# Kernel optimization log

Measured on AMD Instinct MI355X. Metric: run time of the kernel, lower is better.

Reference implementation:

```python
import jax, jax.numpy as jnp
import numpy as np

B, T, IN, HID = 256, 512, 1024, 1024


def setup_inputs() -> dict:
    key = jax.random.key(0)
    ks = jax.random.split(key, 9)
    s = 1.0 / np.sqrt(IN + HID)
    def lin(k):
        kw, kb = jax.random.split(k)
        W = jax.random.uniform(kw, (IN + HID, HID), jnp.float32, -s, s)
        b = jax.random.uniform(kb, (HID,), jnp.float32, -s, s)
        return W, b
    Wf, bf = lin(ks[0])
    Wi, bi = lin(ks[1])
    Wo, bo = lin(ks[2])
    Wc, bc = lin(ks[3])
    x = jax.random.normal(ks[4], (B, T, IN), jnp.float32)
    return {"x": x, "Wf": Wf, "bf": bf, "Wi": Wi, "bi": bi,
            "Wo": Wo, "bo": bo, "Wc": Wc, "bc": bc}


def reference(x, Wf, bf, Wi, bi, Wo, bo, Wc, bc):
    # x: [B, T, IN]; returns final (h, c): each [B, HID]
    batch = x.shape[0]
    hid = Wf.shape[1]

    def step(carry, xt):
        h, c = carry
        comb = jnp.concatenate([xt, h], axis=1)      # [B, IN+HID]
        i = jax.nn.sigmoid(comb @ Wi + bi)
        f = jax.nn.sigmoid(comb @ Wf + bf)
        o = jax.nn.sigmoid(comb @ Wo + bo)
        g = jnp.tanh(comb @ Wc + bc)
        c_next = f * c + i * g
        h_next = o * jnp.tanh(c_next)
        return (h_next, c_next), None

    init = (jnp.zeros((batch, hid), x.dtype), jnp.zeros((batch, hid), x.dtype))
    (h, c), _ = jax.lax.scan(step, init, jnp.swapaxes(x, 0, 1))
    return (h, c)
```

## Files before the change

### kernel.cpp

```cpp
#include <hip/hip_runtime.h>
#include <hip/hip_bf16.h>

#define B_DIM 256
#define T_DIM 512
#define WINT 64
#define IN_DIM 1024
#define HID_DIM 1024
#define BLK 16384

typedef __attribute__((ext_vector_type(8))) short bf16x8;
typedef __attribute__((ext_vector_type(4))) float f32x4;

__device__ __forceinline__ unsigned short f2bf(float v) {
  unsigned int u = __float_as_uint(v);
  unsigned int r = (u + 0x7fffu + ((u >> 16) & 1u)) >> 16;
  return (unsigned short)r;
}
__device__ __forceinline__ float bflo(unsigned u) { return __uint_as_float(u << 16); }
__device__ __forceinline__ float bfhi(unsigned u) { return __uint_as_float(u & 0xffff0000u); }

typedef __attribute__((address_space(3))) unsigned int lds_uint;
typedef const __attribute__((address_space(1))) unsigned int g_uint;
__device__ __forceinline__ void gload_lds16(const void* g, void* l) {
  __builtin_amdgcn_global_load_lds((g_uint*)g, (lds_uint*)l, 16, 0, 0);
}
__device__ __forceinline__ void glds2(const unsigned char* s, unsigned char* d) {
  gload_lds16(s, d);
  gload_lds16(s + 1024, d + 1024);
}

#define WAITVM(N) asm volatile("s_waitcnt vmcnt(" #N ")" ::: "memory")

__global__ void prep_pack_w(const float* __restrict__ Wi, const float* __restrict__ Wf,
                            const float* __restrict__ Wo, const float* __restrict__ Wc,
                            unsigned char* __restrict__ Wp) {
  const int bid = blockIdx.x;
  const int cb = bid >> 4, kc = bid & 15;
  const int tid = threadIdx.x;
  const int col = tid & 63;
  const int g = col >> 4, h_in = col & 15;
  const int kq = tid >> 6;
  const float* W = (g == 0) ? Wi : (g == 1) ? Wf : (g == 2) ? Wo : Wc;
  const float* src = W + (size_t)(kc * 128 + kq * 32) * HID_DIM + cb * 16 + h_in;
  unsigned char* dst = Wp + (size_t)bid * BLK;
  const unsigned int xo = (unsigned int)((col & 7) << 4);
#pragma unroll
  for (int b4 = 0; b4 < 4; ++b4) {
    unsigned short u[8];
#pragma unroll
    for (int j = 0; j < 8; ++j)
      u[j] = f2bf(src[(size_t)(b4 * 8 + j) * HID_DIM]);
    uint4 pk;
    pk.x = (unsigned)u[0] | ((unsigned)u[1] << 16);
    pk.y = (unsigned)u[2] | ((unsigned)u[3] << 16);
    pk.z = (unsigned)u[4] | ((unsigned)u[5] << 16);
    pk.w = (unsigned)u[6] | ((unsigned)u[7] << 16);
    unsigned int byte = ((unsigned int)(col * 256 + kq * 64 + b4 * 16)) ^ xo;
    *(uint4*)(dst + byte) = pk;
  }
}

__global__ void prep_bias(const float* __restrict__ bi, const float* __restrict__ bf_,
                          const float* __restrict__ bo, const float* __restrict__ bc,
                          float* __restrict__ bp) {
  int p = blockIdx.x * 256 + threadIdx.x;
  int cbb = p >> 6, col = p & 63, g = col >> 4, h_in = col & 15;
  const float* b = (g == 0) ? bi : (g == 1) ? bf_ : (g == 2) ? bo : bc;
  bp[p] = b[cbb * 16 + h_in];
}

__global__ void prep_pack_x_win(const float* __restrict__ x,
                                unsigned char* __restrict__ xpw, int t0) {
  const int bid = blockIdx.x;
  const int kc = bid & 7, mb = (bid >> 3) & 3, tw = bid >> 5;
  const int tid = threadIdx.x;
  const int row = tid >> 2, kseg = tid & 3;
  const float* src = x + ((size_t)(mb * 64 + row) * T_DIM + (t0 + tw)) * IN_DIM +
                     kc * 128 + kseg * 32;
  unsigned char* dst = xpw + (size_t)bid * BLK;
  const unsigned int xo = (unsigned)((row & 7) << 4);
#pragma unroll
  for (int c4 = 0; c4 < 4; ++c4) {
    float4 f0 = *(const float4*)(src + c4 * 8);
    float4 f1 = *(const float4*)(src + c4 * 8 + 4);
    uint4 pk;
    pk.x = (unsigned)f2bf(f0.x) | ((unsigned)f2bf(f0.y) << 16);
    pk.y = (unsigned)f2bf(f0.z) | ((unsigned)f2bf(f0.w) << 16);
    pk.z = (unsigned)f2bf(f1.x) | ((unsigned)f2bf(f1.y) << 16);
    pk.w = (unsigned)f2bf(f1.z) | ((unsigned)f2bf(f1.w) << 16);
    *(uint4*)(dst + (((unsigned)(row * 256 + kseg * 64 + c4 * 16)) ^ xo)) = pk;
  }
}

__global__ __launch_bounds__(512, 2) void bulk_gx(
    const unsigned char* __restrict__ xpw, const unsigned char* __restrict__ Wq,
    unsigned char* __restrict__ gxw) {
  extern __shared__ unsigned char ring[];
  const int wg = blockIdx.x;
  const int cb = wg & 63, mb = (wg >> 6) & 3, tg = wg >> 8;
  const int tid = threadIdx.x, lane = tid & 63, w = tid >> 6;
  const int rg = w & 1, cg = (w >> 1) & 1, kh = w >> 2;
  const int fr = lane & 15;
  const unsigned koff2 = (unsigned)((lane >> 4) << 4);
  const int rsub = (lane >> 4) * 4;
  const int cl = cg * 32 + fr;

  bf16x8 Breg[4][2][4];
#pragma unroll
  for (int ci = 0; ci < 4; ++ci)
#pragma unroll
    for (int cbf = 0; cbf < 2; ++cbf)
#pragma unroll
      for (int ks = 0; ks < 4; ++ks) {
        const unsigned c2 = (unsigned)(cl + cbf * 16);
        Breg[ci][cbf][ks] = *(const bf16x8*)(
            Wq + ((size_t)(cb * 16 + kh * 4 + ci) << 14) +
            ((c2 * 256 + (unsigned)ks * 64 + koff2) ^ ((c2 & 7) << 4)));
      }

  float* gates = (float*)ring;
  unsigned char* dstb = ring + w * 2048;

#pragma unroll 1
  for (int i = 0; i < 16; ++i) {
    const int tl = tg * 16 + i;
    const unsigned char* xA =
        xpw + ((size_t)((tl * 4 + mb) * 8)) * BLK + w * 2048 + lane * 16;
    f32x4 acc[2][2] = {{{0.f,0.f,0.f,0.f},{0.f,0.f,0.f,0.f}},
                       {{0.f,0.f,0.f,0.f},{0.f,0.f,0.f,0.f}}};
#pragma unroll
    for (int c = 0; c < 4; ++c) glds2(xA + (size_t)c * BLK, dstb + c * 16384);
#pragma unroll
    for (int kc = 0; kc < 8; ++kc) {
      if (kc <= 4) WAITVM(6);
      else if (kc == 5) WAITVM(4);
      else if (kc == 6) WAITVM(2);
      else WAITVM(0);
      __builtin_amdgcn_s_barrier();
      if ((kc >> 2) == kh) {
        const unsigned char* Ab = ring + (kc & 3) * 16384;
#pragma unroll
        for (int ks = 0; ks < 4; ++ks) {
          const unsigned r0 = (unsigned)(rg * 32 + fr), r1 = r0 + 16;
          const unsigned kb = (unsigned)ks * 64 + koff2;
          bf16x8 a0 = *(const bf16x8*)(Ab + ((r0 * 256 + kb) ^ ((r0 & 7) << 4)));
          bf16x8 a1 = *(const bf16x8*)(Ab + ((r1 * 256 + kb) ^ ((r1 & 7) << 4)));
#pragma unroll
          for (int cbf = 0; cbf < 2; ++cbf) {
            acc[0][cbf] = __builtin_amdgcn_mfma_f32_16x16x32_bf16(
                a0, Breg[kc & 3][cbf][ks], acc[0][cbf], 0, 0, 0);
            acc[1][cbf] = __builtin_amdgcn_mfma_f32_16x16x32_bf16(
                a1, Breg[kc & 3][cbf][ks], acc[1][cbf], 0, 0, 0);
          }
        }
      }
      __builtin_amdgcn_s_barrier();
      if (kc + 4 < 8) glds2(xA + (size_t)(kc + 4) * BLK, dstb + ((kc + 4) & 3) * 16384);
    }
    if (kh == 0) {
#pragma unroll
      for (int rb = 0; rb < 2; ++rb)
#pragma unroll
        for (int cbf = 0; cbf < 2; ++cbf)
#pragma unroll
          for (int j = 0; j < 4; ++j)
            gates[(rg * 32 + rb * 16 + rsub + j) * 65 + cg * 32 + cbf * 16 + fr] =
                acc[rb][cbf][j];
    }
    __syncthreads();
    if (kh == 1) {
#pragma unroll
      for (int rb = 0; rb < 2; ++rb)
#pragma unroll
        for (int cbf = 0; cbf < 2; ++cbf)
#pragma unroll
          for (int j = 0; j < 4; ++j)
            gates[(rg * 32 + rb * 16 + rsub + j) * 65 + cg * 32 + cbf * 16 + fr] +=
                acc[rb][cbf][j];
    }
    __syncthreads();
    {
      const int erow = tid & 63, hb2 = (tid >> 6) * 2;
      uint4 pk;
      unsigned u[4];
#pragma unroll
      for (int g = 0; g < 4; ++g) {
        float lo = gates[erow * 65 + g * 16 + hb2];
        float hi = gates[erow * 65 + g * 16 + hb2 + 1];
        u[g] = (unsigned)f2bf(lo) | ((unsigned)f2bf(hi) << 16);
      }
      pk.x = u[0]; pk.y = u[1]; pk.z = u[2]; pk.w = u[3];
      *(uint4*)(gxw + ((size_t)((tl * 4 + mb) * 64 + cb)) * 8192 + (size_t)tid * 16) = pk;
    }
    __syncthreads();
  }
}

__global__ __launch_bounds__(512, 1) void lstm_seq(
    const unsigned char* __restrict__ gxw, const unsigned char* __restrict__ Wq,
    const float* __restrict__ bp, unsigned char* hring,
    unsigned int* flags, float* cst, float* __restrict__ out, int t0) {
  extern __shared__ unsigned char ring[];
  const int wg = blockIdx.x, mb = wg >> 6, cb = wg & 63;
  const int tid = threadIdx.x, lane = tid & 63, w = tid >> 6;
  const int cg = w & 3, kh = w >> 2;
  const int fr = lane & 15;
  const unsigned koff2 = (unsigned)((lane >> 4) << 4);
  const int rsub = (lane >> 4) * 4;
  const int cl = cg * 16 + fr;

  bf16x8 Breg[4][4];
#pragma unroll
  for (int kcl = 0; kcl < 4; ++kcl)
#pragma unroll
    for (int ks = 0; ks < 4; ++ks)
      Breg[kcl][ks] = *(const bf16x8*)(
          Wq + ((size_t)(cb * 16 + 8 + kh * 4 + kcl) << 14) +
          (((unsigned)cl * 256 + (unsigned)ks * 64 + koff2) ^ ((unsigned)((cl & 7) << 4))));
#pragma unroll
  for (int kcl = 0; kcl < 4; ++kcl)
#pragma unroll
    for (int ks = 0; ks < 4; ++ks)
      asm volatile("" : "+v"(Breg[kcl][ks]));

  const int erow = tid & 63, hb2 = (tid >> 6) * 2;
  const size_t gidx = (size_t)(mb * 64 + erow) * HID_DIM + cb * 16 + hb2;
  float bI[2], bF[2], bO[2], bG[2];
#pragma unroll
  for (int j = 0; j < 2; ++j) {
    bI[j] = bp[cb * 64 + hb2 + j];
    bF[j] = bp[cb * 64 + 16 + hb2 + j];
    bO[j] = bp[cb * 64 + 32 + hb2 + j];
    bG[j] = bp[cb * 64 + 48 + hb2 + j];
  }
  float cr[2] = {0.f, 0.f};
  if (t0 > 0) { float2 c2v = *(const float2*)(cst + gidx); cr[0] = c2v.x; cr[1] = c2v.y; }

  float* gates0 = (float*)ring;
  float* gates1 = (float*)(ring + 32768);

#pragma unroll 1
  for (int tt = 0; tt < WINT; ++tt) {
    const int t = t0 + tt;
#pragma unroll
    for (int kcl = 0; kcl < 4; ++kcl)
#pragma unroll
      for (int ks = 0; ks < 4; ++ks)
        asm volatile("" : "+v"(Breg[kcl][ks]));
    uint4 gxv = *(const uint4*)(gxw + ((size_t)((tt * 4 + mb) * 64 + cb)) * 8192 +
                                (size_t)tid * 16);
    f32x4 acc[4] = {{0.f,0.f,0.f,0.f},{0.f,0.f,0.f,0.f},
                    {0.f,0.f,0.f,0.f},{0.f,0.f,0.f,0.f}};
    if (t > 0) {
      if (w == 0) {
        unsigned int* fl = &flags[mb * 64 + lane];
        while (!__all(__hip_atomic_load(fl, __ATOMIC_RELAXED,
                                        __HIP_MEMORY_SCOPE_AGENT) >= (unsigned)t))
          __builtin_amdgcn_s_sleep(2);
        (void)__hip_atomic_load(fl, __ATOMIC_ACQUIRE,
                                __HIP_MEMORY_SCOPE_AGENT);
      }
      __syncthreads();
      const unsigned char* hA = hring + (size_t)((t + 2) % 3) * 524288 +
                                (size_t)(mb * 8) * BLK + w * 2048 + lane * 16;
#pragma unroll
      for (int c = 0; c < 8; ++c)
        glds2(hA + (size_t)c * BLK, ring + c * 16384 + w * 2048);
#pragma unroll
      for (int kc = 0; kc < 8; ++kc) {
        if (kc == 0) WAITVM(14);
        else if (kc == 1) WAITVM(12);
        else if (kc == 2) WAITVM(10);
        else if (kc == 3) WAITVM(8);
        else if (kc == 4) WAITVM(6);
        else if (kc == 5) WAITVM(4);
        else if (kc == 6) WAITVM(2);
        else WAITVM(0);
        __builtin_amdgcn_s_barrier();
        if ((kc >> 2) == kh) {
          const int kcl = kc & 3;
          const unsigned char* Ab = ring + kc * 16384;
#pragma unroll
          for (int ks = 0; ks < 4; ++ks) {
            const unsigned kb = (unsigned)ks * 64 + koff2;
#pragma unroll
            for (int rb = 0; rb < 4; ++rb) {
              const unsigned r0 = (unsigned)(rb * 16 + fr);
              bf16x8 a0 = *(const bf16x8*)(Ab + ((r0 * 256 + kb) ^ ((r0 & 7) << 4)));
              acc[rb] = __builtin_amdgcn_mfma_f32_16x16x32_bf16(
                  a0, Breg[kcl][ks], acc[rb], 0, 0, 0);
            }
          }
        }
      }
    }
    {
      float* gx_ = (kh == 0) ? gates0 : gates1;
#pragma unroll
      for (int rb = 0; rb < 4; ++rb)
#pragma unroll
        for (int j = 0; j < 4; ++j)
          gx_[(rb * 16 + rsub + j) * 65 + cg * 16 + fr] = acc[rb][j];
    }
    __syncthreads();
    float hv[2];
    {
      unsigned gu0 = gxv.x, gu1 = gxv.y, gu2 = gxv.z, gu3 = gxv.w;
#pragma unroll
      for (int j = 0; j < 2; ++j) {
        int hc = hb2 + j;
        float gx0 = j ? bfhi(gu0) : bflo(gu0);
        float gx1 = j ? bfhi(gu1) : bflo(gu1);
        float gx2 = j ? bfhi(gu2) : bflo(gu2);
        float gx3 = j ? bfhi(gu3) : bflo(gu3);
        float pi = gates0[erow * 65 + hc]      + gates1[erow * 65 + hc]      + bI[j] + gx0;
        float pf = gates0[erow * 65 + 16 + hc] + gates1[erow * 65 + 16 + hc] + bF[j] + gx1;
        float po = gates0[erow * 65 + 32 + hc] + gates1[erow * 65 + 32 + hc] + bO[j] + gx2;
        float pg = gates0[erow * 65 + 48 + hc] + gates1[erow * 65 + 48 + hc] + bG[j] + gx3;
        float ig = 1.f / (1.f + __expf(-pi));
        float fg = 1.f / (1.f + __expf(-pf));
        float og = 1.f / (1.f + __expf(-po));
        float gg = 1.f - 2.f / (1.f + __expf(2.f * pg));
        float cn = fg * cr[j] + ig * gg;
        cr[j] = cn;
        hv[j] = og * (1.f - 2.f / (1.f + __expf(2.f * cn)));
      }
    }
    if (t < T_DIM - 1) {
      int hcg = cb * 16 + hb2;
      int kc2 = hcg >> 7, kp = hcg & 127;
      unsigned byte = ((unsigned)(erow * 256 + kp * 2)) ^ ((unsigned)((erow & 7) << 4));
      unsigned pk = (unsigned)f2bf(hv[0]) | ((unsigned)f2bf(hv[1]) << 16);
      unsigned int* hd = (unsigned int*)(hring + (size_t)(t % 3) * 524288 +
                                         (size_t)(mb * 8 + kc2) * BLK + byte);
      __hip_atomic_store(hd, pk, __ATOMIC_RELAXED, __HIP_MEMORY_SCOPE_AGENT);
    }
    WAITVM(0);
    __syncthreads();
    if (tid == 0 && t < T_DIM - 1)
      __hip_atomic_store(&flags[mb * 64 + cb], (unsigned)(t + 1),
                         __ATOMIC_RELEASE, __HIP_MEMORY_SCOPE_AGENT);
    if (t == T_DIM - 1) {
      *(float2*)(out + gidx) = make_float2(hv[0], hv[1]);
      *(float2*)(out + (size_t)B_DIM * HID_DIM + gidx) = make_float2(cr[0], cr[1]);
    }
  }
  if (t0 + WINT < T_DIM) *(float2*)(cst + gidx) = make_float2(cr[0], cr[1]);
}

extern "C" void kernel_launch(void* const* d_in, const int* in_sizes, int n_in,
                              void* d_out, int out_size, void* d_ws, size_t ws_size,
                              hipStream_t stream) {
  (void)in_sizes; (void)n_in; (void)out_size;
  const float* x   = (const float*)d_in[0];
  const float* Wf_ = (const float*)d_in[1];
  const float* bf_ = (const float*)d_in[2];
  const float* Wi_ = (const float*)d_in[3];
  const float* bi_ = (const float*)d_in[4];
  const float* Wo_ = (const float*)d_in[5];
  const float* bo_ = (const float*)d_in[6];
  const float* Wc_ = (const float*)d_in[7];
  const float* bc_ = (const float*)d_in[8];
  float* out = (float*)d_out;
  unsigned char* ws = (unsigned char*)d_ws;

  unsigned char* Wp = ws;
  size_t off = 16777216;
  float* bp = (float*)(ws + off);                    off += 16384;
  unsigned int* flags = (unsigned int*)(ws + off);   off += 8192;
  unsigned int* consCnt = (unsigned int*)(ws + off); off += 8192;
  (void)consCnt;
  unsigned char* hring = ws + off;                   off += 3 * 524288;
  float* cst = (float*)(ws + off);                   off += 1048576;
  unsigned char* xpw = ws + off;                     off += (size_t)2048 * BLK;
  unsigned char* gxw = ws + off;                     off += (size_t)WINT * 256 * 8192;
  if (ws_size < off) return;

  prep_pack_w<<<1024, 256, 0, stream>>>(Wi_, Wf_, Wo_, Wc_, Wp);
  prep_bias<<<16, 256, 0, stream>>>(bi_, bf_, bo_, bc_, bp);
  hipMemsetAsync(flags, 0, 16384, stream);

  hipFuncSetAttribute((const void*)bulk_gx,
                      hipFuncAttributeMaxDynamicSharedMemorySize, 65536);
  hipFuncSetAttribute((const void*)lstm_seq,
                      hipFuncAttributeMaxDynamicSharedMemorySize, 131072);

  for (int t0 = 0; t0 < T_DIM; t0 += WINT) {
    prep_pack_x_win<<<2048, 256, 0, stream>>>(x, xpw, t0);
    bulk_gx<<<1024, 512, 65536, stream>>>(xpw, Wp, gxw);
    const unsigned char* a_gx = gxw;
    const unsigned char* a_wp = Wp;
    const float* a_bp = bp;
    unsigned char* a_hr = hring;
    unsigned int* a_fl = flags;
    float* a_cs = cst;
    float* a_out = out;
    int a_t0 = t0;
    void* args[] = {&a_gx, &a_wp, &a_bp, &a_hr, &a_fl, &a_cs, &a_out, &a_t0};
    hipLaunchCooperativeKernel((const void*)lstm_seq, dim3(256), dim3(512),
                               args, 131072u, stream);
  }
}
```

Before: 9.463 ms.

## Fuse input-projection GEMM with recurrent steps to overlap next window

Merges the bulk input-projection kernel and the sequential LSTM kernel into one kernel. In each cooperative launch, 256 blocks run the recurrent steps of the current window while another 256 blocks compute the input-gate GEMM for the next window into a double buffer. The window shrinks from 64 to 32 steps, and LDS per block is cut to 64KB so that two blocks can share a CU. This is meant to hide the input-projection cost behind the latency-bound recurrence. The risks are that the co-resident GEMM blocks compete with the recurrent blocks for CU time and memory bandwidth, that the recurrent path now uses a smaller 4-stage LDS ring, and that the extra windows add launch and synchronisation overhead.

```diff
diff --git a/kernel.cpp b/kernel.cpp
--- a/kernel.cpp
+++ b/kernel.cpp
@@ -3,7 +3,8 @@
 
 #define B_DIM 256
 #define T_DIM 512
-#define WINT 64
+#define WINT 32
+#define NWIN 16
 #define IN_DIM 1024
 #define HID_DIM 1024
 #define BLK 16384
@@ -92,44 +93,55 @@
   }
 }
 
-__global__ __launch_bounds__(512, 2) void bulk_gx(
-    const unsigned char* __restrict__ xpw, const unsigned char* __restrict__ Wq,
-    unsigned char* __restrict__ gxw) {
+__global__ __launch_bounds__(512, 4) void lstm_fused(
+    const unsigned char* __restrict__ gxCur, const unsigned char* __restrict__ xpNext,
+    const unsigned char* __restrict__ Wq, const float* __restrict__ bp,
+    unsigned char* __restrict__ gxNext, unsigned char* hring,
+    unsigned int* flags, float* cst, float* __restrict__ out,
+    int t0, int mode) {
   extern __shared__ unsigned char ring[];
-  const int wg = blockIdx.x;
-  const int cb = wg & 63, mb = (wg >> 6) & 3, tg = wg >> 8;
   const int tid = threadIdx.x, lane = tid & 63, w = tid >> 6;
-  const int rg = w & 1, cg = (w >> 1) & 1, kh = w >> 2;
+  const int cg = w & 3, kh = w >> 2;
   const int fr = lane & 15;
   const unsigned koff2 = (unsigned)((lane >> 4) << 4);
   const int rsub = (lane >> 4) * 4;
-  const int cl = cg * 32 + fr;
-
-  bf16x8 Breg[4][2][4];
-#pragma unroll
-  for (int ci = 0; ci < 4; ++ci)
-#pragma unroll
-    for (int cbf = 0; cbf < 2; ++cbf)
-#pragma unroll
-      for (int ks = 0; ks < 4; ++ks) {
-        const unsigned c2 = (unsigned)(cl + cbf * 16);
-        Breg[ci][cbf][ks] = *(const bf16x8*)(
-            Wq + ((size_t)(cb * 16 + kh * 4 + ci) << 14) +
-            ((c2 * 256 + (unsigned)ks * 64 + koff2) ^ ((c2 & 7) << 4)));
-      }
-
-  float* gates = (float*)ring;
-  unsigned char* dstb = ring + w * 2048;
-
-#pragma unroll 1
-  for (int i = 0; i < 16; ++i) {
-    const int tl = tg * 16 + i;
-    const unsigned char* xA =
-        xpw + ((size_t)((tl * 4 + mb) * 8)) * BLK + w * 2048 + lane * 16;
-    f32x4 acc[2][2] = {{{0.f,0.f,0.f,0.f},{0.f,0.f,0.f,0.f}},
-                       {{0.f,0.f,0.f,0.f},{0.f,0.f,0.f,0.f}}};
-#pragma unroll
-    for (int c = 0; c < 4; ++c) glds2(xA + (size_t)c * BLK, dstb + c * 16384);
+  const int cl = cg * 16 + fr;
+
+  bool isSeq; int wg;
+  if (mode == 0) {
+    isSeq = (int)blockIdx.x < 256;
+    wg = isSeq ? (int)blockIdx.x : (int)blockIdx.x - 256;
+  } else {
+    isSeq = (mode == 1);
+    wg = (int)blockIdx.x;
+  }
+  const int mb = (wg >> 6) & 3, cb = wg & 63;
+
+  bf16x8 Breg[4][4];
+  {
+    const int xoff = isSeq ? 8 : 0;
+#pragma unroll
+    for (int kcl = 0; kcl < 4; ++kcl)
+#pragma unroll
+      for (int ks = 0; ks < 4; ++ks)
+        Breg[kcl][ks] = *(const bf16x8*)(
+            Wq + ((size_t)(cb * 16 + xoff + kh * 4 + kcl) << 14) +
+            (((unsigned)cl * 256 + (unsigned)ks * 64 + koff2) ^
+             ((unsigned)((cl & 7) << 4))));
+#pragma unroll
+    for (int kcl = 0; kcl < 4; ++kcl)
+#pragma unroll
+      for (int ks = 0; ks < 4; ++ks)
+        asm volatile("" : "+v"(Breg[kcl][ks]));
+  }
+
+  float* gates0 = (float*)ring;
+  float* gates1 = (float*)(ring + 32768);
+
+  auto phases = [&](const unsigned char* Abase, f32x4* acc) {
+#pragma unroll
+    for (int c = 0; c < 4; ++c)
+      glds2(Abase + (size_t)c * BLK, ring + c * 16384 + w * 2048);
 #pragma unroll
     for (int kc = 0; kc < 8; ++kc) {
       if (kc <= 4) WAITVM(6);
@@ -138,214 +150,156 @@
       else WAITVM(0);
       __builtin_amdgcn_s_barrier();
       if ((kc >> 2) == kh) {
+        const int kcl = kc & 3;
         const unsigned char* Ab = ring + (kc & 3) * 16384;
 #pragma unroll
         for (int ks = 0; ks < 4; ++ks) {
-          const unsigned r0 = (unsigned)(rg * 32 + fr), r1 = r0 + 16;
           const unsigned kb = (unsigned)ks * 64 + koff2;
-          bf16x8 a0 = *(const bf16x8*)(Ab + ((r0 * 256 + kb) ^ ((r0 & 7) << 4)));
-          bf16x8 a1 = *(const bf16x8*)(Ab + ((r1 * 256 + kb) ^ ((r1 & 7) << 4)));
-#pragma unroll
-          for (int cbf = 0; cbf < 2; ++cbf) {
-            acc[0][cbf] = __builtin_amdgcn_mfma_f32_16x16x32_bf16(
-                a0, Breg[kc & 3][cbf][ks], acc[0][cbf], 0, 0, 0);
-            acc[1][cbf] = __builtin_amdgcn_mfma_f32_16x16x32_bf16(
-                a1, Breg[kc & 3][cbf][ks], acc[1][cbf], 0, 0, 0);
+#pragma unroll
+          for (int rb = 0; rb < 4; ++rb) {
+            const unsigned r0 = (unsigned)(rb * 16 + fr);
+            bf16x8 a0 = *(const bf16x8*)(Ab + ((r0 * 256 + kb) ^ ((r0 & 7) << 4)));
+            acc[rb] = __builtin_amdgcn_mfma_f32_16x16x32_bf16(
+                a0, Breg[kcl][ks], acc[rb], 0, 0, 0);
           }
         }
       }
       __builtin_amdgcn_s_barrier();
-      if (kc + 4 < 8) glds2(xA + (size_t)(kc + 4) * BLK, dstb + ((kc + 4) & 3) * 16384);
-    }
-    if (kh == 0) {
-#pragma unroll
-      for (int rb = 0; rb < 2; ++rb)
-#pragma unroll
-        for (int cbf = 0; cbf < 2; ++cbf)
+      if (kc + 4 < 8)
+        glds2(Abase + (size_t)(kc + 4) * BLK, ring + (kc & 3) * 16384 + w * 2048);
+    }
+  };
+
+  if (isSeq) {
+    const int erow = tid & 63, hb2 = (tid >> 6) * 2;
+    const size_t gidx = (size_t)(mb * 64 + erow) * HID_DIM + cb * 16 + hb2;
+    float bI[2], bF[2], bO[2], bG[2];
+#pragma unroll
+    for (int j = 0; j < 2; ++j) {
+      bI[j] = bp[cb * 64 + hb2 + j];
+      bF[j] = bp[cb * 64 + 16 + hb2 + j];
+      bO[j] = bp[cb * 64 + 32 + hb2 + j];
+      bG[j] = bp[cb * 64 + 48 + hb2 + j];
+    }
+    float cr[2] = {0.f, 0.f};
+    if (t0 > 0) { float2 c2v = *(const float2*)(cst + gidx); cr[0] = c2v.x; cr[1] = c2v.y; }
+
+#pragma unroll 1
+    for (int tt = 0; tt < WINT; ++tt) {
+      const int t = t0 + tt;
+#pragma unroll
+      for (int kcl = 0; kcl < 4; ++kcl)
+#pragma unroll
+        for (int ks = 0; ks < 4; ++ks)
+          asm volatile("" : "+v"(Breg[kcl][ks]));
+      uint4 gxv = *(const uint4*)(gxCur + ((size_t)((tt * 4 + mb) * 64 + cb)) * 8192 +
+                                  (size_t)tid * 16);
+      f32x4 acc[4] = {{0.f,0.f,0.f,0.f},{0.f,0.f,0.f,0.f},
+                      {0.f,0.f,0.f,0.f},{0.f,0.f,0.f,0.f}};
+      if (t > 0) {
+        if (w == 0) {
+          unsigned int* fl = &flags[mb * 64 + lane];
+          while (!__all(__hip_atomic_load(fl, __ATOMIC_RELAXED,
+                                          __HIP_MEMORY_SCOPE_AGENT) >= (unsigned)t))
+            __builtin_amdgcn_s_sleep(2);
+          (void)__hip_atomic_load(fl, __ATOMIC_ACQUIRE,
+                                  __HIP_MEMORY_SCOPE_AGENT);
+        }
+        __syncthreads();
+        const unsigned char* hA = hring + (size_t)((t + 2) % 3) * 524288 +
+                                  (size_t)(mb * 8) * BLK + w * 2048 + lane * 16;
+        phases(hA, acc);
+      }
+      {
+        float* g_ = kh ? gates1 : gates0;
+#pragma unroll
+        for (int rb = 0; rb < 4; ++rb)
 #pragma unroll
           for (int j = 0; j < 4; ++j)
-            gates[(rg * 32 + rb * 16 + rsub + j) * 65 + cg * 32 + cbf * 16 + fr] =
-                acc[rb][cbf][j];
-    }
-    __syncthreads();
-    if (kh == 1) {
-#pragma unroll
-      for (int rb = 0; rb < 2; ++rb)
-#pragma unroll
-        for (int cbf = 0; cbf < 2; ++cbf)
+            g_[(rb * 16 + rsub + j) * 65 + cg * 16 + fr] = acc[rb][j];
+      }
+      __syncthreads();
+      float hv[2];
+      {
+        unsigned gu0 = gxv.x, gu1 = gxv.y, gu2 = gxv.z, gu3 = gxv.w;
+#pragma unroll
+        for (int j = 0; j < 2; ++j) {
+          int hc = hb2 + j;
+          float gx0 = j ? bfhi(gu0) : bflo(gu0);
+          float gx1 = j ? bfhi(gu1) : bflo(gu1);
+          float gx2 = j ? bfhi(gu2) : bflo(gu2);
+          float gx3 = j ? bfhi(gu3) : bflo(gu3);
+          float pi = gates0[erow * 65 + hc]      + gates1[erow * 65 + hc]      + bI[j] + gx0;
+          float pf = gates0[erow * 65 + 16 + hc] + gates1[erow * 65 + 16 + hc] + bF[j] + gx1;
+          float po = gates0[erow * 65 + 32 + hc] + gates1[erow * 65 + 32 + hc] + bO[j] + gx2;
+          float pg = gates0[erow * 65 + 48 + hc] + gates1[erow * 65 + 48 + hc] + bG[j] + gx3;
+          float ig = 1.f / (1.f + __expf(-pi));
+          float fg = 1.f / (1.f + __expf(-pf));
+          float og = 1.f / (1.f + __expf(-po));
+          float gg = 1.f - 2.f / (1.f + __expf(2.f * pg));
+          float cn = fg * cr[j] + ig * gg;
+          cr[j] = cn;
+          hv[j] = og * (1.f - 2.f / (1.f + __expf(2.f * cn)));
+        }
+      }
+      if (t < T_DIM - 1) {
+        int hcg = cb * 16 + hb2;
+        int kc2 = hcg >> 7, kp = hcg & 127;
+        unsigned byte = ((unsigned)(erow * 256 + kp * 2)) ^ ((unsigned)((erow & 7) << 4));
+        unsigned pk = (unsigned)f2bf(hv[0]) | ((unsigned)f2bf(hv[1]) << 16);
+        unsigned int* hd = (unsigned int*)(hring + (size_t)(t % 3) * 524288 +
+                                           (size_t)(mb * 8 + kc2) * BLK + byte);
+        __hip_atomic_store(hd, pk, __ATOMIC_RELAXED, __HIP_MEMORY_SCOPE_AGENT);
+      }
+      WAITVM(0);
+      __syncthreads();
+      if (tid == 0 && t < T_DIM - 1)
+        __hip_atomic_store(&flags[mb * 64 + cb], (unsigned)(t + 1),
+                           __ATOMIC_RELEASE, __HIP_MEMORY_SCOPE_AGENT);
+      if (t == T_DIM - 1) {
+        *(float2*)(out + gidx) = make_float2(hv[0], hv[1]);
+        *(float2*)(out + (size_t)B_DIM * HID_DIM + gidx) = make_float2(cr[0], cr[1]);
+      }
+    }
+    if (t0 + WINT < T_DIM) *(float2*)(cst + gidx) = make_float2(cr[0], cr[1]);
+  } else {
+    const int erow = tid & 63, hb2 = (tid >> 6) * 2;
+#pragma unroll 1
+    for (int tl = 0; tl < WINT; ++tl) {
+#pragma unroll
+      for (int kcl = 0; kcl < 4; ++kcl)
+#pragma unroll
+        for (int ks = 0; ks < 4; ++ks)
+          asm volatile("" : "+v"(Breg[kcl][ks]));
+      f32x4 acc[4] = {{0.f,0.f,0.f,0.f},{0.f,0.f,0.f,0.f},
+                      {0.f,0.f,0.f,0.f},{0.f,0.f,0.f,0.f}};
+      const unsigned char* xA = xpNext + ((size_t)((tl * 4 + mb) * 8)) * BLK +
+                                w * 2048 + lane * 16;
+      phases(xA, acc);
+      {
+        float* g_ = kh ? gates1 : gates0;
+#pragma unroll
+        for (int rb = 0; rb < 4; ++rb)
 #pragma unroll
           for (int j = 0; j < 4; ++j)
-            gates[(rg * 32 + rb * 16 + rsub + j) * 65 + cg * 32 + cbf * 16 + fr] +=
-                acc[rb][cbf][j];
-    }
-    __syncthreads();
-    {
-      const int erow = tid & 63, hb2 = (tid >> 6) * 2;
-      uint4 pk;
-      unsigned u[4];
-#pragma unroll
-      for (int g = 0; g < 4; ++g) {
-        float lo = gates[erow * 65 + g * 16 + hb2];
-        float hi = gates[erow * 65 + g * 16 + hb2 + 1];
-        u[g] = (unsigned)f2bf(lo) | ((unsigned)f2bf(hi) << 16);
-      }
-      pk.x = u[0]; pk.y = u[1]; pk.z = u[2]; pk.w = u[3];
-      *(uint4*)(gxw + ((size_t)((tl * 4 + mb) * 64 + cb)) * 8192 + (size_t)tid * 16) = pk;
-    }
-    __syncthreads();
-  }
-}
-
-__global__ __launch_bounds__(512, 1) void lstm_seq(
-    const unsigned char* __restrict__ gxw, const unsigned char* __restrict__ Wq,
-    const float* __restrict__ bp, unsigned char* hring,
-    unsigned int* flags, float* cst, float* __restrict__ out, int t0) {
-  extern __shared__ unsigned char ring[];
-  const int wg = blockIdx.x, mb = wg >> 6, cb = wg & 63;
-  const int tid = threadIdx.x, lane = tid & 63, w = tid >> 6;
-  const int cg = w & 3, kh = w >> 2;
-  const int fr = lane & 15;
-  const unsigned koff2 = (unsigned)((lane >> 4) << 4);
-  const int rsub = (lane >> 4) * 4;
-  const int cl = cg * 16 + fr;
-
-  bf16x8 Breg[4][4];
-#pragma unroll
-  for (int kcl = 0; kcl < 4; ++kcl)
-#pragma unroll
-    for (int ks = 0; ks < 4; ++ks)
-      Breg[kcl][ks] = *(const bf16x8*)(
-          Wq + ((size_t)(cb * 16 + 8 + kh * 4 + kcl) << 14) +
-          (((unsigned)cl * 256 + (unsigned)ks * 64 + koff2) ^ ((unsigned)((cl & 7) << 4))));
-#pragma unroll
-  for (int kcl = 0; kcl < 4; ++kcl)
-#pragma unroll
-    for (int ks = 0; ks < 4; ++ks)
-      asm volatile("" : "+v"(Breg[kcl][ks]));
-
-  const int erow = tid & 63, hb2 = (tid >> 6) * 2;
-  const size_t gidx = (size_t)(mb * 64 + erow) * HID_DIM + cb * 16 + hb2;
-  float bI[2], bF[2], bO[2], bG[2];
-#pragma unroll
-  for (int j = 0; j < 2; ++j) {
-    bI[j] = bp[cb * 64 + hb2 + j];
-    bF[j] = bp[cb * 64 + 16 + hb2 + j];
-    bO[j] = bp[cb * 64 + 32 + hb2 + j];
-    bG[j] = bp[cb * 64 + 48 + hb2 + j];
-  }
-  float cr[2] = {0.f, 0.f};
-  if (t0 > 0) { float2 c2v = *(const float2*)(cst + gidx); cr[0] = c2v.x; cr[1] = c2v.y; }
-
-  float* gates0 = (float*)ring;
-  float* gates1 = (float*)(ring + 32768);
-
-#pragma unroll 1
-  for (int tt = 0; tt < WINT; ++tt) {
-    const int t = t0 + tt;
-#pragma unroll
-    for (int kcl = 0; kcl < 4; ++kcl)
-#pragma unroll
-      for (int ks = 0; ks < 4; ++ks)
-        asm volatile("" : "+v"(Breg[kcl][ks]));
-    uint4 gxv = *(const uint4*)(gxw + ((size_t)((tt * 4 + mb) * 64 + cb)) * 8192 +
-                                (size_t)tid * 16);
-    f32x4 acc[4] = {{0.f,0.f,0.f,0.f},{0.f,0.f,0.f,0.f},
-                    {0.f,0.f,0.f,0.f},{0.f,0.f,0.f,0.f}};
-    if (t > 0) {
-      if (w == 0) {
-        unsigned int* fl = &flags[mb * 64 + lane];
-        while (!__all(__hip_atomic_load(fl, __ATOMIC_RELAXED,
-                                        __HIP_MEMORY_SCOPE_AGENT) >= (unsigned)t))
-          __builtin_amdgcn_s_sleep(2);
-        (void)__hip_atomic_load(fl, __ATOMIC_ACQUIRE,
-                                __HIP_MEMORY_SCOPE_AGENT);
+            g_[(rb * 16 + rsub + j) * 65 + cg * 16 + fr] = acc[rb][j];
       }
       __syncthreads();
-      const unsigned char* hA = hring + (size_t)((t + 2) % 3) * 524288 +
-                                (size_t)(mb * 8) * BLK + w * 2048 + lane * 16;
-#pragma unroll
-      for (int c = 0; c < 8; ++c)
-        glds2(hA + (size_t)c * BLK, ring + c * 16384 + w * 2048);
-#pragma unroll
-      for (int kc = 0; kc < 8; ++kc) {
-        if (kc == 0) WAITVM(14);
-        else if (kc == 1) WAITVM(12);
-        else if (kc == 2) WAITVM(10);
-        else if (kc == 3) WAITVM(8);
-        else if (kc == 4) WAITVM(6);
-        else if (kc == 5) WAITVM(4);
-        else if (kc == 6) WAITVM(2);
-        else WAITVM(0);
-        __builtin_amdgcn_s_barrier();
-        if ((kc >> 2) == kh) {
-          const int kcl = kc & 3;
-          const unsigned char* Ab = ring + kc * 16384;
-#pragma unroll
-          for (int ks = 0; ks < 4; ++ks) {
-            const unsigned kb = (unsigned)ks * 64 + koff2;
-#pragma unroll
-            for (int rb = 0; rb < 4; ++rb) {
-              const unsigned r0 = (unsigned)(rb * 16 + fr);
-              bf16x8 a0 = *(const bf16x8*)(Ab + ((r0 * 256 + kb) ^ ((r0 & 7) << 4)));
-              acc[rb] = __builtin_amdgcn_mfma_f32_16x16x32_bf16(
-                  a0, Breg[kcl][ks], acc[rb], 0, 0, 0);
-            }
-          }
+      {
+        unsigned u[4];
+#pragma unroll
+        for (int g = 0; g < 4; ++g) {
+          float lo = gates0[erow * 65 + g * 16 + hb2] + gates1[erow * 65 + g * 16 + hb2];
+          float hi = gates0[erow * 65 + g * 16 + hb2 + 1] + gates1[erow * 65 + g * 16 + hb2 + 1];
+          u[g] = (unsigned)f2bf(lo) | ((unsigned)f2bf(hi) << 16);
         }
-      }
-    }
-    {
-      float* gx_ = (kh == 0) ? gates0 : gates1;
-#pragma unroll
-      for (int rb = 0; rb < 4; ++rb)
-#pragma unroll
-        for (int j = 0; j < 4; ++j)
-          gx_[(rb * 16 + rsub + j) * 65 + cg * 16 + fr] = acc[rb][j];
-    }
-    __syncthreads();
-    float hv[2];
-    {
-      unsigned gu0 = gxv.x, gu1 = gxv.y, gu2 = gxv.z, gu3 = gxv.w;
-#pragma unroll
-      for (int j = 0; j < 2; ++j) {
-        int hc = hb2 + j;
-        float gx0 = j ? bfhi(gu0) : bflo(gu0);
-        float gx1 = j ? bfhi(gu1) : bflo(gu1);
-        float gx2 = j ? bfhi(gu2) : bflo(gu2);
-        float gx3 = j ? bfhi(gu3) : bflo(gu3);
-        float pi = gates0[erow * 65 + hc]      + gates1[erow * 65 + hc]      + bI[j] + gx0;
-        float pf = gates0[erow * 65 + 16 + hc] + gates1[erow * 65 + 16 + hc] + bF[j] + gx1;
-        float po = gates0[erow * 65 + 32 + hc] + gates1[erow * 65 + 32 + hc] + bO[j] + gx2;
-        float pg = gates0[erow * 65 + 48 + hc] + gates1[erow * 65 + 48 + hc] + bG[j] + gx3;
-        float ig = 1.f / (1.f + __expf(-pi));
-        float fg = 1.f / (1.f + __expf(-pf));
-        float og = 1.f / (1.f + __expf(-po));
-        float gg = 1.f - 2.f / (1.f + __expf(2.f * pg));
-        float cn = fg * cr[j] + ig * gg;
-        cr[j] = cn;
-        hv[j] = og * (1.f - 2.f / (1.f + __expf(2.f * cn)));
-      }
-    }
-    if (t < T_DIM - 1) {
-      int hcg = cb * 16 + hb2;
-      int kc2 = hcg >> 7, kp = hcg & 127;
-      unsigned byte = ((unsigned)(erow * 256 + kp * 2)) ^ ((unsigned)((erow & 7) << 4));
-      unsigned pk = (unsigned)f2bf(hv[0]) | ((unsigned)f2bf(hv[1]) << 16);
-      unsigned int* hd = (unsigned int*)(hring + (size_t)(t % 3) * 524288 +
-                                         (size_t)(mb * 8 + kc2) * BLK + byte);
-      __hip_atomic_store(hd, pk, __ATOMIC_RELAXED, __HIP_MEMORY_SCOPE_AGENT);
-    }
-    WAITVM(0);
-    __syncthreads();
-    if (tid == 0 && t < T_DIM - 1)
-      __hip_atomic_store(&flags[mb * 64 + cb], (unsigned)(t + 1),
-                         __ATOMIC_RELEASE, __HIP_MEMORY_SCOPE_AGENT);
-    if (t == T_DIM - 1) {
-      *(float2*)(out + gidx) = make_float2(hv[0], hv[1]);
-      *(float2*)(out + (size_t)B_DIM * HID_DIM + gidx) = make_float2(cr[0], cr[1]);
-    }
-  }
-  if (t0 + WINT < T_DIM) *(float2*)(cst + gidx) = make_float2(cr[0], cr[1]);
+        uint4 pk; pk.x = u[0]; pk.y = u[1]; pk.z = u[2]; pk.w = u[3];
+        *(uint4*)(gxNext + ((size_t)((tl * 4 + mb) * 64 + cb)) * 8192 +
+                  (size_t)tid * 16) = pk;
+      }
+      __syncthreads();
+    }
+  }
 }
 
 extern "C" void kernel_launch(void* const* d_in, const int* in_sizes, int n_in,
@@ -368,36 +322,70 @@
   size_t off = 16777216;
   float* bp = (float*)(ws + off);                    off += 16384;
   unsigned int* flags = (unsigned int*)(ws + off);   off += 8192;
-  unsigned int* consCnt = (unsigned int*)(ws + off); off += 8192;
-  (void)consCnt;
+  off += 8192;
   unsigned char* hring = ws + off;                   off += 3 * 524288;
   float* cst = (float*)(ws + off);                   off += 1048576;
-  unsigned char* xpw = ws + off;                     off += (size_t)2048 * BLK;
-  unsigned char* gxw = ws + off;                     off += (size_t)WINT * 256 * 8192;
+  unsigned char* xpw0 = ws + off;                    off += (size_t)WINT * 32 * BLK;
+  unsigned char* xpw1 = ws + off;                    off += (size_t)WINT * 32 * BLK;
+  unsigned char* gxw0 = ws + off;                    off += (size_t)WINT * 256 * 8192;
+  unsigned char* gxw1 = ws + off;                    off += (size_t)WINT * 256 * 8192;
   if (ws_size < off) return;
 
   prep_pack_w<<<1024, 256, 0, stream>>>(Wi_, Wf_, Wo_, Wc_, Wp);
   prep_bias<<<16, 256, 0, stream>>>(bi_, bf_, bo_, bc_, bp);
-  hipMemsetAsync(flags, 0, 16384, stream);
-
-  hipFuncSetAttribute((const void*)bulk_gx,
+  hipMemsetAsync(flags, 0, 8192, stream);
+
+  hipFuncSetAttribute((const void*)lstm_fused,
                       hipFuncAttributeMaxDynamicSharedMemorySize, 65536);
-  hipFuncSetAttribute((const void*)lstm_seq,
-                      hipFuncAttributeMaxDynamicSharedMemorySize, 131072);
-
-  for (int t0 = 0; t0 < T_DIM; t0 += WINT) {
-    prep_pack_x_win<<<2048, 256, 0, stream>>>(x, xpw, t0);
-    bulk_gx<<<1024, 512, 65536, stream>>>(xpw, Wp, gxw);
-    const unsigned char* a_gx = gxw;
+  int nb = 0;
+  hipOccupancyMaxActiveBlocksPerMultiprocessor(&nb, (const void*)lstm_fused, 512, 65536);
+  const bool canFuse = (nb >= 2);
+
+  prep_pack_x_win<<<WINT * 32, 256, 0, stream>>>(x, xpw0, 0);
+  {
+    const unsigned char* a_gc = gxw1;
+    const unsigned char* a_xp = xpw0;
     const unsigned char* a_wp = Wp;
     const float* a_bp = bp;
+    unsigned char* a_gn = gxw0;
+    lstm_fused<<<256, 512, 65536, stream>>>(a_gc, a_xp, a_wp, a_bp, a_gn, hring,
+                                            flags, cst, out, 0, 2);
+  }
+
+  for (int wnd = 0; wnd < NWIN; ++wnd) {
+    const int t0v = wnd * WINT;
+    unsigned char* gxC = (wnd & 1) ? gxw1 : gxw0;
+    unsigned char* gxN = (wnd & 1) ? gxw0 : gxw1;
+    unsigned char* xpN = (wnd & 1) ? xpw0 : xpw1;
+    if (wnd < NWIN - 1)
+      prep_pack_x_win<<<WINT * 32, 256, 0, stream>>>(x, xpN, (wnd + 1) * WINT);
+
+    const unsigned char* a_gc = gxC;
+    const unsigned char* a_xp = xpN;
+    const unsigned char* a_wp = Wp;
+    const float* a_bp = bp;
+    unsigned char* a_gn = gxN;
     unsigned char* a_hr = hring;
     unsigned int* a_fl = flags;
     float* a_cs = cst;
     float* a_out = out;
-    int a_t0 = t0;
-    void* args[] = {&a_gx, &a_wp, &a_bp, &a_hr, &a_fl, &a_cs, &a_out, &a_t0};
-    hipLaunchCooperativeKernel((const void*)lstm_seq, dim3(256), dim3(512),
-                               args, 131072u, stream);
-  }
-}
+    int a_t0 = t0v;
+
+    if (canFuse && wnd < NWIN - 1) {
+      int a_mode = 0;
+      void* args[] = {&a_gc, &a_xp, &a_wp, &a_bp, &a_gn, &a_hr, &a_fl, &a_cs,
+                      &a_out, &a_t0, &a_mode};
+      hipLaunchCooperativeKernel((const void*)lstm_fused, dim3(512), dim3(512),
+                                 args, 65536u, stream);
+    } else {
+      int a_mode = 1;
+      void* args[] = {&a_gc, &a_xp, &a_wp, &a_bp, &a_gn, &a_hr, &a_fl, &a_cs,
+                      &a_out, &a_t0, &a_mode};
+      hipLaunchCooperativeKernel((const void*)lstm_fused, dim3(256), dim3(512),
+                                 args, 65536u, stream);
+      if (wnd < NWIN - 1)
+        lstm_fused<<<256, 512, 65536, stream>>>(a_gc, a_xp, a_wp, a_bp, a_gn,
+                                                a_hr, a_fl, a_cs, a_out, a_t0, 2);
+    }
+  }
+}
```

New measurement: 13.07 ms. 38.1% more time.
